# Kernel optimization log

Hardware: AMD Instinct MI355X
Metric: run time of the kernel (lower is better)

## Reference

```python
import jax, jax.numpy as jnp
import numpy as np

N = 100000   # nodes
E = 1600000  # edges
D = 128      # input_dim == hidden_dim
L = 4        # n_layers
G = 128      # num graphs
NC = 10      # n_classes
EPS = 1e-5


def setup_inputs() -> dict:
    key = jax.random.key(0)
    ks = jax.random.split(key, 12)
    x = jax.random.normal(ks[0], (N, D), jnp.float32)
    edge_index = jax.random.randint(ks[1], (2, E), 0, N, dtype=jnp.int64)
    batch = jnp.sort(jax.random.randint(ks[2], (N,), 0, G, dtype=jnp.int64))
    s = 1.0 / np.sqrt(D)
    conv_w = jax.random.normal(ks[3], (L, D, D), jnp.float32) * s
    conv_b = jnp.zeros((L, D), jnp.float32)
    gn_weight = jnp.ones((L, D), jnp.float32)
    gn_bias = jnp.zeros((L, D), jnp.float32)
    gn_mean_scale = jnp.ones((L, D), jnp.float32)
    dense_w1 = jax.random.normal(ks[4], (D, D), jnp.float32) * s
    dense_b1 = jnp.zeros((D,), jnp.float32)
    bn_gamma = jnp.ones((D,), jnp.float32)
    bn_beta = jnp.zeros((D,), jnp.float32)
    bn_mean = jnp.zeros((D,), jnp.float32)   # running stats (eval mode)
    bn_var = jnp.ones((D,), jnp.float32)
    dense_w2 = jax.random.normal(ks[5], (D, NC), jnp.float32) * s
    dense_b2 = jnp.zeros((NC,), jnp.float32)
    return dict(x=x, edge_index=edge_index, batch=batch, conv_w=conv_w,
                conv_b=conv_b, gn_weight=gn_weight, gn_bias=gn_bias,
                gn_mean_scale=gn_mean_scale, dense_w1=dense_w1, dense_b1=dense_b1,
                bn_gamma=bn_gamma, bn_beta=bn_beta, bn_mean=bn_mean, bn_var=bn_var,
                dense_w2=dense_w2, dense_b2=dense_b2)


def _graph_norm(x, batch, counts, weight, bias, mean_scale):
    # PyG GraphNorm: (x - alpha*mean) / sqrt(var + eps) * weight + bias, per graph
    mean = jax.ops.segment_sum(x, batch, num_segments=G) / counts        # [G, D]
    sub = x - mean_scale * mean[batch]                                    # [N, D]
    var = jax.ops.segment_sum(sub * sub, batch, num_segments=G) / counts  # [G, D]
    return weight * sub * jax.lax.rsqrt(var + EPS)[batch] + bias


def reference(x, edge_index, batch, conv_w, conv_b, gn_weight, gn_bias,
              gn_mean_scale, dense_w1, dense_b1, bn_gamma, bn_beta,
              bn_mean, bn_var, dense_w2, dense_b2):
    # GCNConv normalization with self-loops (symmetric D^-1/2 (A+I) D^-1/2)
    loop = jnp.arange(N, dtype=edge_index.dtype)
    src = jnp.concatenate([edge_index[0], loop])
    dst = jnp.concatenate([edge_index[1], loop])
    deg = jax.ops.segment_sum(jnp.ones((E + N,), x.dtype), dst, num_segments=N)
    dis = jax.lax.rsqrt(deg)  # deg >= 1 due to self-loops
    nrm = (dis[src] * dis[dst])[:, None]                                  # [E+N, 1]
    counts = jax.ops.segment_sum(jnp.ones((N, 1), x.dtype), batch, num_segments=G)

    x_res = x  # input_dim == hidden_dim -> no input projection
    for i in range(L):
        h = x @ conv_w[i]                                # [N, D]
        h = jax.ops.segment_sum(h[src] * nrm, dst, num_segments=N) + conv_b[i]
        h = _graph_norm(h, batch, counts, gn_weight[i], gn_bias[i], gn_mean_scale[i])
        h = jax.nn.elu(h)
        # dropout: identity in eval mode
        x = h + x_res
        x_res = x

    pooled = jax.ops.segment_sum(x, batch, num_segments=G)  # global_add_pool [G, D]
    z = pooled @ dense_w1 + dense_b1
    z = bn_gamma * (z - bn_mean) * jax.lax.rsqrt(bn_var + EPS) + bn_beta
    z = jax.nn.relu(z)
    z = z @ dense_w2 + dense_b2
    return (x, z)
```

## Files before the change

### kernel.cpp

```cpp
#include <hip/hip_runtime.h>
#include <stdint.h>

#define N_NODES 100000
#define N_PAD   100032
#define N_EDGES 1600000
#define DIM 128
#define NLAYERS 4
#define NGRAPH 128
#define NCLS 10
#define EPSV 1e-5f
#define NSLOT 32
#define POOL_PARTS 8

#define BIN_SHIFT 9
#define NBUCKET ((N_NODES + 511) >> 9)
#define P1_EPB 4096
#define P1_BLOCKS ((N_EDGES + P1_EPB - 1) / P1_EPB)

typedef __attribute__((ext_vector_type(8))) short short8_t;
typedef __attribute__((ext_vector_type(4))) float float4_t;


__device__ __forceinline__ float bf_lo(uint32_t u) { return __uint_as_float(u << 16); }
__device__ __forceinline__ float bf_hi(uint32_t u) { return __uint_as_float(u & 0xffff0000u); }
__device__ __forceinline__ uint32_t f2bf_rne(float f) {
    uint32_t x = __float_as_uint(f);
    return (x + 0x7fffu + ((x >> 16) & 1u)) >> 16;
}
__device__ __forceinline__ uint32_t pack_bf2(float a, float b) {
    return f2bf_rne(a) | (f2bf_rne(b) << 16);
}
__device__ __forceinline__ float4 unpack4(uint2 u) {
    return make_float4(bf_lo(u.x), bf_hi(u.x), bf_lo(u.y), bf_hi(u.y));
}
__device__ __forceinline__ float ub0(uint32_t u) { return (float)( u        & 0xffu); }
__device__ __forceinline__ float ub1(uint32_t u) { return (float)((u >>  8) & 0xffu); }
__device__ __forceinline__ float ub2(uint32_t u) { return (float)((u >> 16) & 0xffu); }
__device__ __forceinline__ float ub3(uint32_t u) { return (float)( u >> 24        ); }
__device__ __forceinline__ float elu_neg(float x) { return __expf(x) - 1.f; }


__global__ void k_node_meta(const int* __restrict__ batch, int* __restrict__ gstart,
                            int* __restrict__ bcnt, float* __restrict__ pooled) {
    int i = blockIdx.x * blockDim.x + threadIdx.x;
    if (i < NBUCKET) bcnt[i] = 0;
    if (i < NGRAPH * DIM) pooled[i] = 0.f;
    if (i >= N_NODES) return;
    int b = batch[i];
    if (i == 0) {
        for (int g = 0; g <= b; g++) gstart[g] = 0;
    } else {
        int bp = batch[i - 1];
        for (int g = bp + 1; g <= b; g++) gstart[g] = i;
    }
    if (i == N_NODES - 1) {
        for (int g = b + 1; g <= NGRAPH; g++) gstart[g] = N_NODES;
    }
}

__global__ __launch_bounds__(256) void k_bhist(const int* __restrict__ ei, int* __restrict__ bcnt) {
    __shared__ int hist[NBUCKET];
    int t = threadIdx.x;
    for (int i = t; i < NBUCKET; i += 256) hist[i] = 0;
    __syncthreads();
    int e0 = blockIdx.x * P1_EPB;
    int e1 = e0 + P1_EPB; if (e1 > N_EDGES) e1 = N_EDGES;
    for (int e = e0 + t; e < e1; e += 256) atomicAdd(&hist[ei[N_EDGES + e] >> BIN_SHIFT], 1);
    __syncthreads();
    for (int i = t; i < NBUCKET; i += 256) if (hist[i]) atomicAdd(&bcnt[i], hist[i]);
}

__global__ __launch_bounds__(256) void k_bscan(const int* __restrict__ bcnt,
                                               int* __restrict__ bucket_off, int* __restrict__ bcur) {
    __shared__ int s[256];
    int t = threadIdx.x;
    int v = (t < NBUCKET) ? bcnt[t] : 0;
    s[t] = v; __syncthreads();
    for (int off = 1; off < 256; off <<= 1) {
        int a = (t >= off) ? s[t - off] : 0;
        __syncthreads();
        s[t] += a;
        __syncthreads();
    }
    if (t < NBUCKET) { bucket_off[t] = s[t] - v; bcur[t] = s[t] - v; }
    if (t == 0) bucket_off[NBUCKET] = s[255];
}

__global__ __launch_bounds__(256) void k_bin_edges(const int* __restrict__ ei,
                                                   int* __restrict__ bcur,
                                                   int2* __restrict__ binned) {
    __shared__ int hist[NBUCKET];
    __shared__ int base[NBUCKET];
    int t = threadIdx.x;
    int e0 = blockIdx.x * P1_EPB;
    int e1 = e0 + P1_EPB; if (e1 > N_EDGES) e1 = N_EDGES;
    for (int i = t; i < NBUCKET; i += 256) hist[i] = 0;
    __syncthreads();
    int myrank[P1_EPB / 256];
    int cnt = 0;
    for (int e = e0 + t; e < e1; e += 256) {
        int d = ei[N_EDGES + e];
        myrank[cnt++] = atomicAdd(&hist[d >> BIN_SHIFT], 1);
    }
    __syncthreads();
    for (int i = t; i < NBUCKET; i += 256) base[i] = atomicAdd(&bcur[i], hist[i]);
    __syncthreads();
    cnt = 0;
    for (int e = e0 + t; e < e1; e += 256) {
        int s = ei[e];
        int d = ei[N_EDGES + e];
        binned[base[d >> BIN_SHIFT] + myrank[cnt++]] = make_int2(s, d);
    }
}

__global__ __launch_bounds__(256) void k_bucket_build(const int2* __restrict__ binned,
                                                      const int* __restrict__ bucket_off,
                                                      int* __restrict__ rowoff,
                                                      float* __restrict__ dis,
                                                      int* __restrict__ psrc) {
    __shared__ int cnt[512];
    __shared__ int sa[512];
    __shared__ int sb[512];
    int b = blockIdx.x;
    int t = threadIdx.x;
    int n0 = b << BIN_SHIFT;
    int j0 = bucket_off[b], j1 = bucket_off[b + 1];
    cnt[t] = 0; cnt[t + 256] = 0;
    __syncthreads();
    for (int j = j0 + t; j < j1; j += 256) atomicAdd(&cnt[binned[j].y & 511], 1);
    __syncthreads();
    sa[t] = cnt[t]; sa[t + 256] = cnt[t + 256];
    __syncthreads();
    int* A = sa; int* B = sb;
    for (int off = 1; off < 512; off <<= 1) {
        int i0 = t, i1 = t + 256;
        B[i0] = A[i0] + ((i0 >= off) ? A[i0 - off] : 0);
        B[i1] = A[i1] + ((i1 >= off) ? A[i1 - off] : 0);
        __syncthreads();
        int* tmp = A; A = B; B = tmp;
    }
    for (int i = t; i < 512; i += 256) {
        int n = n0 + i;
        if (n < N_NODES) {
            rowoff[n] = j0 + A[i] - cnt[i];
            dis[n] = rsqrtf((float)(1 + cnt[i]));
        }
    }
    if (b == NBUCKET - 1 && t == 0) rowoff[N_NODES] = N_EDGES;
    for (int idx = t; idx < 512 * NSLOT; idx += 256) {
        int i = idx >> 5, k = idx & (NSLOT - 1);
        int n = n0 + i;
        if (n < N_NODES && k >= cnt[i]) psrc[(size_t)n * NSLOT + k] = (k == cnt[i]) ? n : N_NODES;
    }
}

__global__ __launch_bounds__(256) void k_scatter(const int2* __restrict__ binned,
                                                 const float* __restrict__ dis,
                                                 const int* __restrict__ rowoff,
                                                 const int* __restrict__ bucket_off,
                                                 int2* __restrict__ csc,
                                                 int* __restrict__ psrc) {
    __shared__ int lcur[512];
    int b = blockIdx.x;
    int t = threadIdx.x;
    lcur[t] = 0; lcur[t + 256] = 0;
    __syncthreads();
    int j0 = bucket_off[b], j1 = bucket_off[b + 1];
    for (int j = j0 + t; j < j1; j += 256) {
        int2 sd = binned[j];
        float w = dis[sd.x] * dis[sd.y];
        int rank = atomicAdd(&lcur[sd.y & 511], 1);
        csc[rowoff[sd.y] + rank] = make_int2(sd.x, __float_as_int(w));
        if (rank < NSLOT) psrc[(size_t)sd.y * NSLOT + rank] = sd.x;
    }
}

__global__ void k_cast_w(const float* __restrict__ W, uint32_t* __restrict__ Wt) {
    int i = blockIdx.x * blockDim.x + threadIdx.x;
    if (i >= NLAYERS * DIM * 64) return;
    int l = i / (DIM * 64);
    int n = (i / 64) % DIM;
    int ku = i % 64;
    const float* Wl = W + (size_t)l * DIM * DIM;
    float w0 = Wl[(2 * ku) * DIM + n];
    float w1 = Wl[(2 * ku + 1) * DIM + n];
    Wt[i] = pack_bf2(w0, w1);
}


__device__ __forceinline__ void gemm_phase(const uint32_t (*atile)[68], const uint32_t* __restrict__ Wt,
                                           uint8_t (*ctile8)[132], float* rmaxl,
                                           uint8_t* __restrict__ H8,
                                           float* __restrict__ hsd, const float* __restrict__ dis,
                                           int blk, int t) {
    int wid = t >> 6;
    int lane = t & 63;
    int quad = lane >> 4;
    int s15 = lane & 15;

    float4_t acc[8];
#pragma unroll
    for (int i = 0; i < 8; i++) acc[i] = (float4_t){0.f, 0.f, 0.f, 0.f};

#pragma unroll
    for (int kk = 0; kk < 4; kk++) {
        uint4 au = *(const uint4*)&atile[wid * 16 + s15][quad * 4 + kk * 16];
        short8_t a = __builtin_bit_cast(short8_t, au);
#pragma unroll
        for (int nt = 0; nt < 8; nt++) {
            uint4 bu = *(const uint4*)(Wt + (size_t)(nt * 16 + s15) * 64 + kk * 16 + quad * 4);
            short8_t b = __builtin_bit_cast(short8_t, bu);
            acc[nt] = __builtin_amdgcn_mfma_f32_16x16x32_bf16(a, b, acc[nt], 0, 0, 0);
        }
    }
    __syncthreads();

    float sinv[4];
#pragma unroll
    for (int r = 0; r < 4; r++) {
        float m = fabsf(acc[0][r]);
#pragma unroll
        for (int nt = 1; nt < 8; nt++) m = fmaxf(m, fabsf(acc[nt][r]));
        m = fmaxf(m, __shfl_xor(m, 1));
        m = fmaxf(m, __shfl_xor(m, 2));
        m = fmaxf(m, __shfl_xor(m, 4));
        m = fmaxf(m, __shfl_xor(m, 8));
        if (s15 == 0) rmaxl[wid * 16 + quad * 4 + r] = m;
        sinv[r] = (m > 0.f) ? 127.f / m : 0.f;
    }
#pragma unroll
    for (int nt = 0; nt < 8; nt++) {
#pragma unroll
        for (int r = 0; r < 4; r++) {
            int qv = (int)fmaf(acc[nt][r], sinv[r], 128.5f);
            ctile8[wid * 16 + quad * 4 + r][nt * 16 + s15] = (uint8_t)qv;
        }
    }
    __syncthreads();
    uint8_t* Hb = H8 + (size_t)blk * 64 * 128;
    float* Hsb = hsd + (size_t)blk * 64;
#pragma unroll
    for (int i = 0; i < 8; i++) {
        int idx = t + 256 * i;
        int row = idx >> 5, cu = idx & 31;
        uint32_t v = *(const uint32_t*)&ctile8[row][cu * 4];
        ((uint32_t*)Hb)[(size_t)row * 32 + cu] = v;
        if (cu == 0) {
            size_t gr = (size_t)blk * 64 + row;
            float dv = (gr < N_NODES) ? dis[gr] : 0.f;
            Hsb[row] = rmaxl[row] * (1.f / 127.f) * dv;
        }
    }
}

#define GEMM_SMEM \
    __shared__ __align__(16) char smem[64 * 68 * 4]; \
    uint32_t (*atile)[68] = (uint32_t(*)[68])smem; \
    uint8_t (*ctile8)[132] = (uint8_t(*)[132])smem; \
    float* rmaxl = (float*)(smem + 64 * 132);

__global__ __launch_bounds__(256) void k_gemm0(const float* __restrict__ X, const uint32_t* __restrict__ Wt,
                                               uint8_t* __restrict__ H8, float* __restrict__ hsd,
                                               const float* __restrict__ dis) {
    GEMM_SMEM
    int t = threadIdx.x;
    size_t row0 = (size_t)blockIdx.x * 64;
#pragma unroll
    for (int i = 0; i < 8; i++) {
        int idx = t + 256 * i;
        int row = idx >> 5, q = idx & 31;
        size_t gr = row0 + row;
        uint2 p = make_uint2(0u, 0u);
        if (gr < N_NODES) {
            float4 v = ((const float4*)(X + gr * DIM))[q];
            p.x = pack_bf2(v.x, v.y);
            p.y = pack_bf2(v.z, v.w);
        }
        *(uint2*)&atile[row][q * 2] = p;
    }
    __syncthreads();
    gemm_phase(atile, Wt, ctile8, rmaxl, H8, hsd, dis, blockIdx.x, t);
}

template <bool RBF>
__global__ __launch_bounds__(256) void k_norm_gemm(const uint32_t* __restrict__ A, const int* __restrict__ batch,
                                                   const float* __restrict__ amean, const float* __restrict__ rstd,
                                                   const float* __restrict__ gw, const float* __restrict__ gb,
                                                   const void* __restrict__ res, uint32_t* __restrict__ res_out,
                                                   const uint32_t* __restrict__ Wt,
                                                   uint8_t* __restrict__ H8, float* __restrict__ hsd,
                                                   const float* __restrict__ dis) {
    GEMM_SMEM
    int t = threadIdx.x;
    size_t row0 = (size_t)blockIdx.x * 64;
#pragma unroll
    for (int i = 0; i < 8; i++) {
        int idx = t + 256 * i;
        int row = idx >> 5, q = idx & 31;
        size_t gr = row0 + row;
        uint2 p = make_uint2(0u, 0u);
        if (gr < N_NODES) {
            int g = batch[gr];
            float4 v = unpack4(((const uint2*)(A + gr * 64))[q]);
            float4 am = ((const float4*)amean)[g * 32 + q];
            float4 rs = ((const float4*)rstd)[g * 32 + q];
            float4 w = ((const float4*)gw)[q];
            float4 b = ((const float4*)gb)[q];
            float4 r;
            if (RBF) r = unpack4(((const uint2*)((const uint32_t*)res + gr * 64))[q]);
            else     r = ((const float4*)res)[gr * 32 + q];
            float4 o;
            o.x = w.x * (v.x - am.x) * rs.x + b.x;
            o.y = w.y * (v.y - am.y) * rs.y + b.y;
            o.z = w.z * (v.z - am.z) * rs.z + b.z;
            o.w = w.w * (v.w - am.w) * rs.w + b.w;
            o.x = ((o.x > 0.f) ? o.x : elu_neg(o.x)) + r.x;
            o.y = ((o.y > 0.f) ? o.y : elu_neg(o.y)) + r.y;
            o.z = ((o.z > 0.f) ? o.z : elu_neg(o.z)) + r.z;
            o.w = ((o.w > 0.f) ? o.w : elu_neg(o.w)) + r.w;
            p.x = pack_bf2(o.x, o.y);
            p.y = pack_bf2(o.z, o.w);
            ((uint2*)(res_out + gr * 64))[q] = p;
        }
        *(uint2*)&atile[row][q * 2] = p;
    }
    __syncthreads();
    gemm_phase(atile, Wt, ctile8, rmaxl, H8, hsd, dis, blockIdx.x, t);
}


#define ACC8(WS, U) \
    acc[0] += WS * ub0(U.x); acc[1] += WS * ub1(U.x); \
    acc[2] += WS * ub2(U.x); acc[3] += WS * ub3(U.x); \
    acc[4] += WS * ub0(U.y); acc[5] += WS * ub1(U.y); \
    acc[6] += WS * ub2(U.y); acc[7] += WS * ub3(U.y);

__global__ __launch_bounds__(256, 4) void k_aggregate(const uint8_t* __restrict__ H8,
                                                      const float* __restrict__ hsd,
                                                      const int* __restrict__ psrc,
                                                      const int2* __restrict__ csc,
                                                      const int* __restrict__ rowoff,
                                                      const float* __restrict__ dis,
                                                      const float* __restrict__ bias,
                                                      uint32_t* __restrict__ Out) {
    int wid = threadIdx.x >> 6;
    int lane = threadIdx.x & 63;
    uint32_t hq = (uint32_t)((lane >> 4) & 1);
    uint32_t s  = (uint32_t)(lane & 15);
    uint32_t n  = (uint32_t)blockIdx.x * 8u + ((uint32_t)wid << 1) + (uint32_t)(lane >> 5);
    uint32_t s8 = s << 3;

    float dd = dis[n];
    int b0 = rowoff[n], b1 = rowoff[n + 1];
    const int4* P = (const int4*)(psrc + ((size_t)n << 5) + (hq << 4));
    int4 pa = P[0], pb = P[1], pc = P[2], pd = P[3];

    float h0 = hsd[(uint32_t)pa.x], h1 = hsd[(uint32_t)pa.y];
    float h2 = hsd[(uint32_t)pa.z], h3 = hsd[(uint32_t)pa.w];
    float h4 = hsd[(uint32_t)pb.x], h5 = hsd[(uint32_t)pb.y];
    float h6 = hsd[(uint32_t)pb.z], h7 = hsd[(uint32_t)pb.w];
    uint2 u0 = *(const uint2*)(H8 + (((uint32_t)pa.x << 7) | s8));
    uint2 u1 = *(const uint2*)(H8 + (((uint32_t)pa.y << 7) | s8));
    uint2 u2 = *(const uint2*)(H8 + (((uint32_t)pa.z << 7) | s8));
    uint2 u3 = *(const uint2*)(H8 + (((uint32_t)pa.w << 7) | s8));
    uint2 u4 = *(const uint2*)(H8 + (((uint32_t)pb.x << 7) | s8));
    uint2 u5 = *(const uint2*)(H8 + (((uint32_t)pb.y << 7) | s8));
    uint2 u6 = *(const uint2*)(H8 + (((uint32_t)pb.z << 7) | s8));
    uint2 u7 = *(const uint2*)(H8 + (((uint32_t)pb.w << 7) | s8));

    float acc[8];
#pragma unroll
    for (int k = 0; k < 8; k++) acc[k] = 0.f;

    ACC8(h0, u0); ACC8(h1, u1); ACC8(h2, u2); ACC8(h3, u3);
    ACC8(h4, u4); ACC8(h5, u5); ACC8(h6, u6); ACC8(h7, u7);

    float h8  = hsd[(uint32_t)pc.x], h9  = hsd[(uint32_t)pc.y];
    float h10 = hsd[(uint32_t)pc.z], h11 = hsd[(uint32_t)pc.w];
    float h12 = hsd[(uint32_t)pd.x], h13 = hsd[(uint32_t)pd.y];
    float h14 = hsd[(uint32_t)pd.z], h15 = hsd[(uint32_t)pd.w];
    uint2 u8  = *(const uint2*)(H8 + (((uint32_t)pc.x << 7) | s8));
    uint2 u9  = *(const uint2*)(H8 + (((uint32_t)pc.y << 7) | s8));
    uint2 u10 = *(const uint2*)(H8 + (((uint32_t)pc.z << 7) | s8));
    uint2 u11 = *(const uint2*)(H8 + (((uint32_t)pc.w << 7) | s8));
    uint2 u12 = *(const uint2*)(H8 + (((uint32_t)pd.x << 7) | s8));
    uint2 u13 = *(const uint2*)(H8 + (((uint32_t)pd.y << 7) | s8));
    uint2 u14 = *(const uint2*)(H8 + (((uint32_t)pd.z << 7) | s8));
    uint2 u15 = *(const uint2*)(H8 + (((uint32_t)pd.w << 7) | s8));

    ACC8(h8, u8);  ACC8(h9, u9);  ACC8(h10, u10); ACC8(h11, u11);
    ACC8(h12, u12); ACC8(h13, u13); ACC8(h14, u14); ACC8(h15, u15);

    float offs = ((h0 + h1) + (h2 + h3)) + ((h4 + h5) + (h6 + h7))
               + ((h8 + h9) + (h10 + h11)) + ((h12 + h13) + (h14 + h15));

    if (b1 - b0 >= NSLOT) {
        float wsf = (hq == 0) ? hsd[n] : 0.f;
        uint2 uu = *(const uint2*)(H8 + ((n << 7) | s8));
        ACC8(wsf, uu);
        offs += wsf;
        for (int j = b0 + NSLOT + (int)hq; j < b1; j += 2) {
            uint32_t sx = (uint32_t)csc[j].x;
            float w = hsd[sx];
            uint2 u = *(const uint2*)(H8 + ((sx << 7) | s8));
            ACC8(w, u);
            offs += w;
        }
    }

#pragma unroll
    for (int k = 0; k < 8; k++) acc[k] += __shfl_xor(acc[k], 16);
    offs += __shfl_xor(offs, 16);

    float corr = -128.f * offs;
    float a0 = hq ? acc[4] : acc[0];
    float a1 = hq ? acc[5] : acc[1];
    float a2 = hq ? acc[6] : acc[2];
    float a3 = hq ? acc[7] : acc[3];
    float4 bb = ((const float4*)bias)[(s << 1) | hq];
    uint2 ov;
    ov.x = pack_bf2(fmaf(dd, a0 + corr, bb.x), fmaf(dd, a1 + corr, bb.y));
    ov.y = pack_bf2(fmaf(dd, a2 + corr, bb.z), fmaf(dd, a3 + corr, bb.w));
    *(uint2*)(Out + ((n << 6) | (s << 2) | (hq << 1))) = ov;
}

__global__ __launch_bounds__(512) void k_stats(const uint32_t* __restrict__ A, const int* __restrict__ gstart,
                                               const float* __restrict__ mscale,
                                               float* __restrict__ amean, float* __restrict__ rstd) {
    __shared__ float L1[8][DIM];
    __shared__ float L2[8][DIM];
    int g = blockIdx.x;
    int t = threadIdx.x;
    int f2 = t & 63;
    int p = t >> 6;
    int s0 = gstart[g], s1 = gstart[g + 1];
    float sa = 0.f, sb = 0.f, qa = 0.f, qb = 0.f;
    for (int n = s0 + p; n < s1; n += 8) {
        uint32_t u = A[(size_t)n * 64 + f2];
        float a = bf_lo(u), b = bf_hi(u);
        sa += a; qa += a * a;
        sb += b; qb += b * b;
    }
    L1[p][2 * f2] = sa; L1[p][2 * f2 + 1] = sb;
    L2[p][2 * f2] = qa; L2[p][2 * f2 + 1] = qb;
    __syncthreads();
    if (t < DIM) {
        float s = 0.f, s2 = 0.f;
#pragma unroll
        for (int i = 0; i < 8; i++) { s += L1[i][t]; s2 += L2[i][t]; }
        int cnt = s1 - s0;
        float inv = (cnt > 0) ? 1.0f / (float)cnt : 0.f;
        float m = s * inv;
        float a = mscale[t];
        float var = s2 * inv - (2.f * a - a * a) * m * m;
        amean[g * DIM + t] = a * m;
        rstd[g * DIM + t] = rsqrtf(var + EPSV);
    }
}

__global__ __launch_bounds__(512) void k_norm_pool(const uint32_t* __restrict__ A,
                                                   const uint32_t* __restrict__ resb,
                                                   const int* __restrict__ gstart,
                                                   const float* __restrict__ amean, const float* __restrict__ rstd,
                                                   const float* __restrict__ gw, const float* __restrict__ gb,
                                                   float* __restrict__ outx, float* __restrict__ pooled) {
    __shared__ float L[8][DIM];
    int g = blockIdx.x >> 3;
    int part = blockIdx.x & 7;
    int t = threadIdx.x;
    int f2 = t & 63;
    int p = t >> 6;
    int slice = part * 8 + p;
    int s0 = gstart[g], s1 = gstart[g + 1];
    float am0 = amean[g * DIM + 2 * f2], am1 = amean[g * DIM + 2 * f2 + 1];
    float rs0 = rstd[g * DIM + 2 * f2],  rs1 = rstd[g * DIM + 2 * f2 + 1];
    float w0_ = gw[2 * f2], w1_ = gw[2 * f2 + 1];
    float b0_ = gb[2 * f2], b1_ = gb[2 * f2 + 1];
    float p0 = 0.f, p1 = 0.f;
    for (int n = s0 + slice; n < s1; n += 64) {
        uint32_t u = A[(size_t)n * 64 + f2];
        uint32_t ur = resb[(size_t)n * 64 + f2];
        float a = bf_lo(u), b = bf_hi(u);
        float r0 = bf_lo(ur), r1 = bf_hi(ur);
        float o0 = w0_ * (a - am0) * rs0 + b0_;
        float o1 = w1_ * (b - am1) * rs1 + b1_;
        o0 = ((o0 > 0.f) ? o0 : elu_neg(o0)) + r0;
        o1 = ((o1 > 0.f) ? o1 : elu_neg(o1)) + r1;
        ((float2*)(outx + (size_t)n * DIM))[f2] = make_float2(o0, o1);
        p0 += o0; p1 += o1;
    }
    L[p][2 * f2] = p0; L[p][2 * f2 + 1] = p1;
    __syncthreads();
    if (t < DIM) {
        float s = 0.f;
#pragma unroll
        for (int i = 0; i < 8; i++) s += L[i][t];
        if (s != 0.f) atomicAdd(&pooled[g * DIM + t], s);
    }
}

__global__ __launch_bounds__(128) void k_head(const float* __restrict__ pooled,
                                              const float* __restrict__ w1, const float* __restrict__ b1,
                                              const float* __restrict__ gamma, const float* __restrict__ beta,
                                              const float* __restrict__ rmean, const float* __restrict__ rvar,
                                              const float* __restrict__ w2, const float* __restrict__ b2,
                                              float* __restrict__ zout) {
    __shared__ float sz[DIM];
    int g = blockIdx.x, t = threadIdx.x;
    const float* sp = pooled + g * DIM;
    float acc = b1[t];
#pragma unroll 8
    for (int k = 0; k < DIM; k++) acc += sp[k] * w1[k * DIM + t];
    acc = gamma[t] * (acc - rmean[t]) * rsqrtf(rvar[t] + EPSV) + beta[t];
    sz[t] = fmaxf(acc, 0.f);
    __syncthreads();
    if (t < NCLS) {
        float a2 = b2[t];
#pragma unroll 8
        for (int k = 0; k < DIM; k++) a2 += sz[k] * w2[k * NCLS + t];
        zout[g * NCLS + t] = a2;
    }
}


extern "C" void kernel_launch(void* const* d_in, const int* in_sizes, int n_in,
                              void* d_out, int out_size, void* d_ws, size_t ws_size,
                              hipStream_t stream) {
    const float* x_in   = (const float*)d_in[0];
    const int*   ei     = (const int*)d_in[1];
    const int*   batch  = (const int*)d_in[2];
    const float* conv_w = (const float*)d_in[3];
    const float* conv_b = (const float*)d_in[4];
    const float* gn_w   = (const float*)d_in[5];
    const float* gn_b   = (const float*)d_in[6];
    const float* gn_ms  = (const float*)d_in[7];
    const float* w1     = (const float*)d_in[8];
    const float* b1     = (const float*)d_in[9];
    const float* bng    = (const float*)d_in[10];
    const float* bnb    = (const float*)d_in[11];
    const float* bnm    = (const float*)d_in[12];
    const float* bnv    = (const float*)d_in[13];
    const float* w2     = (const float*)d_in[14];
    const float* b2     = (const float*)d_in[15];

    float* out_x = (float*)d_out;
    float* out_z = out_x + (size_t)N_NODES * DIM;

    char* ws = (char*)d_ws;
    size_t off = 0;
    auto alloc = [&](size_t bytes) -> void* {
        void* p = ws + off;
        off += (bytes + 255) / 256 * 256;
        return p;
    };
    uint8_t* h8      = (uint8_t*)alloc(sizeof(uint8_t) * (size_t)N_PAD * 128);
    float*   hsd     = (float*)alloc(sizeof(float) * (size_t)N_PAD);
    uint32_t* agg    = (uint32_t*)alloc(sizeof(uint32_t) * (size_t)N_NODES * 64);
    uint32_t* resb   = (uint32_t*)alloc(sizeof(uint32_t) * (size_t)N_NODES * 64);
    int2*  csc       = (int2*)alloc(sizeof(int2) * (size_t)N_EDGES);
    int2*  binned    = (int2*)alloc(sizeof(int2) * (size_t)N_EDGES);
    int*   psrc      = (int*)alloc(sizeof(int) * (size_t)N_NODES * NSLOT);
    uint32_t* wt     = (uint32_t*)alloc(sizeof(uint32_t) * NLAYERS * DIM * 64);
    float* dis       = (float*)alloc(sizeof(float) * N_NODES);
    int*   rowoff    = (int*)alloc(sizeof(int) * (N_NODES + 1));
    int*   bcnt      = (int*)alloc(sizeof(int) * NBUCKET);
    int*   boffb     = (int*)alloc(sizeof(int) * (NBUCKET + 1));
    int*   bcur      = (int*)alloc(sizeof(int) * NBUCKET);
    int*   gstart    = (int*)alloc(sizeof(int) * (NGRAPH + 1));
    float* amean     = (float*)alloc(sizeof(float) * NGRAPH * DIM);
    float* rstd      = (float*)alloc(sizeof(float) * NGRAPH * DIM);
    float* pooled    = (float*)alloc(sizeof(float) * NGRAPH * DIM);

    k_node_meta<<<(N_NODES + 255) / 256, 256, 0, stream>>>(batch, gstart, bcnt, pooled);
    k_bhist<<<P1_BLOCKS, 256, 0, stream>>>(ei, bcnt);
    k_bscan<<<1, 256, 0, stream>>>(bcnt, boffb, bcur);
    k_bin_edges<<<P1_BLOCKS, 256, 0, stream>>>(ei, bcur, binned);
    k_bucket_build<<<NBUCKET, 256, 0, stream>>>(binned, boffb, rowoff, dis, psrc);
    k_scatter<<<NBUCKET, 256, 0, stream>>>(binned, dis, rowoff, boffb, csc, psrc);
    k_cast_w<<<(NLAYERS * DIM * 64 + 255) / 256, 256, 0, stream>>>(conv_w, wt);

    k_gemm0<<<N_PAD / 64, 256, 0, stream>>>(x_in, wt, h8, hsd, dis);
    for (int l = 0; l < NLAYERS; l++) {
        k_aggregate<<<N_NODES / 8, 256, 0, stream>>>(h8, hsd, psrc, csc, rowoff, dis,
                                                     conv_b + (size_t)l * DIM, agg);
        k_stats<<<NGRAPH, 512, 0, stream>>>(agg, gstart, gn_ms + (size_t)l * DIM, amean, rstd);
        if (l == 0) {
            k_norm_gemm<false><<<N_PAD / 64, 256, 0, stream>>>(agg, batch, amean, rstd, gn_w, gn_b,
                                                               (const void*)x_in, resb,
                                                               wt + (size_t)1 * DIM * 64, h8, hsd, dis);
        } else if (l < NLAYERS - 1) {
            k_norm_gemm<true><<<N_PAD / 64, 256, 0, stream>>>(agg, batch, amean, rstd,
                                                              gn_w + (size_t)l * DIM, gn_b + (size_t)l * DIM,
                                                              (const void*)resb, resb,
                                                              wt + (size_t)(l + 1) * DIM * 64, h8, hsd, dis);
        } else {
            k_norm_pool<<<NGRAPH * POOL_PARTS, 512, 0, stream>>>(agg, resb, gstart, amean, rstd,
                                                                 gn_w + (size_t)l * DIM, gn_b + (size_t)l * DIM,
                                                                 out_x, pooled);
            k_head<<<NGRAPH, 128, 0, stream>>>(pooled, w1, b1, bng, bnb, bnm, bnv, w2, b2, out_z);
        }
    }
}
```

Measured before the change: 724.3 us.

## Make GEMM kernels persistent with register prefetch of next tile

The GEMM and norm+GEMM kernels become grid-stride persistent loops over 64-row tiles with a fixed grid. Each block loads the next tile's inputs into registers before running the GEMM phase on the current tile, so global load latency overlaps compute. This costs extra registers, an extra barrier per tile, and a smaller launch grid, which may reduce occupancy.

Measured after the change: 808.1 us. 1.12x slower.

```diff
diff --git a/kernel.cpp b/kernel.cpp
--- a/kernel.cpp
+++ b/kernel.cpp
@@ -11,6 +11,8 @@
 #define EPSV 1e-5f
 #define NSLOT 32
 #define POOL_PARTS 8
+#define NTILE (N_PAD / 64)
+#define GEMM_GRID 782
 
 #define BIN_SHIFT 9
 #define NBUCKET ((N_NODES + 511) >> 9)
@@ -264,22 +266,36 @@
                                                const float* __restrict__ dis) {
     GEMM_SMEM
     int t = threadIdx.x;
-    size_t row0 = (size_t)blockIdx.x * 64;
-#pragma unroll
-    for (int i = 0; i < 8; i++) {
-        int idx = t + 256 * i;
-        int row = idx >> 5, q = idx & 31;
-        size_t gr = row0 + row;
-        uint2 p = make_uint2(0u, 0u);
-        if (gr < N_NODES) {
-            float4 v = ((const float4*)(X + gr * DIM))[q];
-            p.x = pack_bf2(v.x, v.y);
-            p.y = pack_bf2(v.z, v.w);
-        }
-        *(uint2*)&atile[row][q * 2] = p;
-    }
-    __syncthreads();
-    gemm_phase(atile, Wt, ctile8, rmaxl, H8, hsd, dis, blockIdx.x, t);
+    float4 pf[8];
+    int tile = blockIdx.x;
+    auto prefetch = [&](int tl) {
+#pragma unroll
+        for (int i = 0; i < 8; i++) {
+            int idx = t + 256 * i;
+            int row = idx >> 5, q = idx & 31;
+            size_t gr = (size_t)tl * 64 + row;
+            pf[i] = (gr < N_NODES) ? ((const float4*)(X + gr * DIM))[q]
+                                   : make_float4(0.f, 0.f, 0.f, 0.f);
+        }
+    };
+    prefetch(tile);
+    while (tile < NTILE) {
+        int cur = tile;
+        tile += GEMM_GRID;
+#pragma unroll
+        for (int i = 0; i < 8; i++) {
+            int idx = t + 256 * i;
+            int row = idx >> 5, q = idx & 31;
+            uint2 p;
+            p.x = pack_bf2(pf[i].x, pf[i].y);
+            p.y = pack_bf2(pf[i].z, pf[i].w);
+            *(uint2*)&atile[row][q * 2] = p;
+        }
+        __syncthreads();
+        if (tile < NTILE) prefetch(tile);
+        gemm_phase(atile, Wt, ctile8, rmaxl, H8, hsd, dis, cur, t);
+        __syncthreads();
+    }
 }
 
 template <bool RBF>
@@ -292,40 +308,70 @@
                                                    const float* __restrict__ dis) {
     GEMM_SMEM
     int t = threadIdx.x;
-    size_t row0 = (size_t)blockIdx.x * 64;
-#pragma unroll
-    for (int i = 0; i < 8; i++) {
-        int idx = t + 256 * i;
-        int row = idx >> 5, q = idx & 31;
-        size_t gr = row0 + row;
-        uint2 p = make_uint2(0u, 0u);
-        if (gr < N_NODES) {
-            int g = batch[gr];
-            float4 v = unpack4(((const uint2*)(A + gr * 64))[q]);
-            float4 am = ((const float4*)amean)[g * 32 + q];
-            float4 rs = ((const float4*)rstd)[g * 32 + q];
-            float4 w = ((const float4*)gw)[q];
-            float4 b = ((const float4*)gb)[q];
-            float4 r;
-            if (RBF) r = unpack4(((const uint2*)((const uint32_t*)res + gr * 64))[q]);
-            else     r = ((const float4*)res)[gr * 32 + q];
-            float4 o;
-            o.x = w.x * (v.x - am.x) * rs.x + b.x;
-            o.y = w.y * (v.y - am.y) * rs.y + b.y;
-            o.z = w.z * (v.z - am.z) * rs.z + b.z;
-            o.w = w.w * (v.w - am.w) * rs.w + b.w;
-            o.x = ((o.x > 0.f) ? o.x : elu_neg(o.x)) + r.x;
-            o.y = ((o.y > 0.f) ? o.y : elu_neg(o.y)) + r.y;
-            o.z = ((o.z > 0.f) ? o.z : elu_neg(o.z)) + r.z;
-            o.w = ((o.w > 0.f) ? o.w : elu_neg(o.w)) + r.w;
-            p.x = pack_bf2(o.x, o.y);
-            p.y = pack_bf2(o.z, o.w);
-            ((uint2*)(res_out + gr * 64))[q] = p;
-        }
-        *(uint2*)&atile[row][q * 2] = p;
-    }
-    __syncthreads();
-    gemm_phase(atile, Wt, ctile8, rmaxl, H8, hsd, dis, blockIdx.x, t);
+    uint2 pa[8];
+    uint2 pr2[8];
+    float4 pr4[8];
+    int   pg[8];
+    int tile = blockIdx.x;
+    auto prefetch = [&](int tl) {
+#pragma unroll
+        for (int i = 0; i < 8; i++) {
+            int idx = t + 256 * i;
+            int row = idx >> 5, q = idx & 31;
+            size_t gr = (size_t)tl * 64 + row;
+            if (gr < N_NODES) {
+                pg[i] = batch[gr];
+                pa[i] = ((const uint2*)(A + gr * 64))[q];
+                if (RBF) pr2[i] = ((const uint2*)((const uint32_t*)res + gr * 64))[q];
+                else     pr4[i] = ((const float4*)res)[gr * 32 + q];
+            } else {
+                pg[i] = 0;
+                pa[i] = make_uint2(0u, 0u);
+                if (RBF) pr2[i] = make_uint2(0u, 0u);
+                else     pr4[i] = make_float4(0.f, 0.f, 0.f, 0.f);
+            }
+        }
+    };
+    prefetch(tile);
+    while (tile < NTILE) {
+        int cur = tile;
+        tile += GEMM_GRID;
+#pragma unroll
+        for (int i = 0; i < 8; i++) {
+            int idx = t + 256 * i;
+            int row = idx >> 5, q = idx & 31;
+            size_t gr = (size_t)cur * 64 + row;
+            uint2 p = make_uint2(0u, 0u);
+            if (gr < N_NODES) {
+                int g = pg[i];
+                float4 v = unpack4(pa[i]);
+                float4 am = ((const float4*)amean)[g * 32 + q];
+                float4 rs = ((const float4*)rstd)[g * 32 + q];
+                float4 w = ((const float4*)gw)[q];
+                float4 b = ((const float4*)gb)[q];
+                float4 r;
+                if (RBF) r = unpack4(pr2[i]);
+                else     r = pr4[i];
+                float4 o;
+                o.x = w.x * (v.x - am.x) * rs.x + b.x;
+                o.y = w.y * (v.y - am.y) * rs.y + b.y;
+                o.z = w.z * (v.z - am.z) * rs.z + b.z;
+                o.w = w.w * (v.w - am.w) * rs.w + b.w;
+                o.x = ((o.x > 0.f) ? o.x : elu_neg(o.x)) + r.x;
+                o.y = ((o.y > 0.f) ? o.y : elu_neg(o.y)) + r.y;
+                o.z = ((o.z > 0.f) ? o.z : elu_neg(o.z)) + r.z;
+                o.w = ((o.w > 0.f) ? o.w : elu_neg(o.w)) + r.w;
+                p.x = pack_bf2(o.x, o.y);
+                p.y = pack_bf2(o.z, o.w);
+                ((uint2*)(res_out + gr * 64))[q] = p;
+            }
+            *(uint2*)&atile[row][q * 2] = p;
+        }
+        __syncthreads();
+        if (tile < NTILE) prefetch(tile);
+        gemm_phase(atile, Wt, ctile8, rmaxl, H8, hsd, dis, cur, t);
+        __syncthreads();
+    }
 }
 
 
@@ -579,20 +625,20 @@
     k_scatter<<<NBUCKET, 256, 0, stream>>>(binned, dis, rowoff, boffb, csc, psrc);
     k_cast_w<<<(NLAYERS * DIM * 64 + 255) / 256, 256, 0, stream>>>(conv_w, wt);
 
-    k_gemm0<<<N_PAD / 64, 256, 0, stream>>>(x_in, wt, h8, hsd, dis);
+    k_gemm0<<<GEMM_GRID, 256, 0, stream>>>(x_in, wt, h8, hsd, dis);
     for (int l = 0; l < NLAYERS; l++) {
         k_aggregate<<<N_NODES / 8, 256, 0, stream>>>(h8, hsd, psrc, csc, rowoff, dis,
                                                      conv_b + (size_t)l * DIM, agg);
         k_stats<<<NGRAPH, 512, 0, stream>>>(agg, gstart, gn_ms + (size_t)l * DIM, amean, rstd);
         if (l == 0) {
-            k_norm_gemm<false><<<N_PAD / 64, 256, 0, stream>>>(agg, batch, amean, rstd, gn_w, gn_b,
-                                                               (const void*)x_in, resb,
-                                                               wt + (size_t)1 * DIM * 64, h8, hsd, dis);
+            k_norm_gemm<false><<<GEMM_GRID, 256, 0, stream>>>(agg, batch, amean, rstd, gn_w, gn_b,
+                                                              (const void*)x_in, resb,
+                                                              wt + (size_t)1 * DIM * 64, h8, hsd, dis);
         } else if (l < NLAYERS - 1) {
-            k_norm_gemm<true><<<N_PAD / 64, 256, 0, stream>>>(agg, batch, amean, rstd,
-                                                              gn_w + (size_t)l * DIM, gn_b + (size_t)l * DIM,
-                                                              (const void*)resb, resb,
-                                                              wt + (size_t)(l + 1) * DIM * 64, h8, hsd, dis);
+            k_norm_gemm<true><<<GEMM_GRID, 256, 0, stream>>>(agg, batch, amean, rstd,
+                                                             gn_w + (size_t)l * DIM, gn_b + (size_t)l * DIM,
+                                                             (const void*)resb, resb,
+                                                             wt + (size_t)(l + 1) * DIM * 64, h8, hsd, dis);
         } else {
             k_norm_pool<<<NGRAPH * POOL_PARTS, 512, 0, stream>>>(agg, resb, gstart, amean, rstd,
                                                                  gn_w + (size_t)l * DIM, gn_b + (size_t)l * DIM,
```
